# Performance work log

Measured on AMD Instinct MI355X. Metric: run time of the kernel, lower is better.

## Reference

```python
import jax, jax.numpy as jnp
import numpy as np

N, V, E = 65536, 2048, 1024
TEMPERATURE = 0.5
EPS = 1e-10
LOG_PARAM_Q = -2.995732273553991


def _l2_normalize(x, axis):
    # matches torch F.normalize(p=2): x / max(||x||, 1e-12)
    n = jnp.sqrt(jnp.sum(x * x, axis=axis, keepdims=True))
    return x / jnp.maximum(n, 1e-12)


def setup_inputs() -> dict:
    key = jax.random.key(0)
    k1, k2, k3 = jax.random.split(key, 3)
    z = jax.random.normal(k1, (N, E), dtype=jnp.float32)
    emb_weight = jax.random.normal(k2, (V, E), dtype=jnp.float32)
    U = jax.random.uniform(k3, (N, V), dtype=jnp.float32)
    return {"z": z, "emb_weight": emb_weight, "U": U}


def reference(z, emb_weight, U):
    kappa_q = jnp.exp(jnp.float32(LOG_PARAM_Q)) + jnp.float32(1.0)
    zn = _l2_normalize(z, axis=1)              # [N, E]
    emb = _l2_normalize(emb_weight, axis=1)    # [V, E]
    # logit = -distances = kappa_q * z @ emb.T
    logit = kappa_q * jnp.matmul(zn, emb.T)    # [N, V]
    # gumbel-softmax sample (training branch)
    g = -jnp.log(-jnp.log(U + EPS) + EPS)
    tokens = jax.nn.softmax((logit + g) / TEMPERATURE, axis=-1)  # [N, V]
    z_q = jnp.matmul(tokens, emb)              # [N, E]
    return (tokens, z_q)
```

## Files before the change

kernel.cpp:

```cpp
#include <hip/hip_runtime.h>
#include <hip/hip_bf16.h>
#include <stdint.h>

typedef short bf16x8 __attribute__((ext_vector_type(8)));
typedef float floatx4 __attribute__((ext_vector_type(4)));

#define N_ROWS 65536
#define V_DIM 2048
#define E_DIM 1024

__device__ __forceinline__ short f2bf(float x) {
  union { float f; uint32_t u; } c; c.f = x;
  uint32_t r = (c.u + 0x7FFFu + ((c.u >> 16) & 1u)) >> 16;
  return (short)(uint16_t)r;
}
__device__ __forceinline__ float bf16f(short b) {
  union { uint32_t u; float f; } c; c.u = ((uint32_t)(uint16_t)b) << 16;
  return c.f;
}

__device__ __forceinline__ float wave_sum(float v) {
#pragma unroll
  for (int o = 32; o > 0; o >>= 1) v += __shfl_xor(v, o);
  return v;
}
__device__ __forceinline__ float wave_max(float v) {
#pragma unroll
  for (int o = 32; o > 0; o >>= 1) v = fmaxf(v, __shfl_xor(v, o));
  return v;
}

__device__ __forceinline__ void gll16(const short* g, short* l) {
  __builtin_amdgcn_global_load_lds(
      (const __attribute__((address_space(1))) void*)g,
      (__attribute__((address_space(3))) void*)l, 16, 0, 0);
}

#define FRAG(base, R, c) \
  (*(const bf16x8*)((const char*)(base) + ((R) << 7) + (((((c) >> 3) ^ ((R) & 7))) << 4)))

__global__ __launch_bounds__(256) void k_norm_emb(const float* __restrict__ W,
                                                  short* __restrict__ embn,
                                                  short* __restrict__ embnT) {
  const int v = blockIdx.x;
  const int t = threadIdx.x;
  const int w = t >> 6, l = t & 63;
  const float4 val = *(const float4*)&W[(size_t)v * E_DIM + t * 4];
  float ss = val.x * val.x + val.y * val.y + val.z * val.z + val.w * val.w;
  ss = wave_sum(ss);
  __shared__ float red[4];
  if (l == 0) red[w] = ss;
  __syncthreads();
  ss = red[0] + red[1] + red[2] + red[3];
  const float inv = 1.0f / fmaxf(sqrtf(ss), 1e-12f);
  short4 o;
  o.x = f2bf(val.x * inv);
  o.y = f2bf(val.y * inv);
  o.z = f2bf(val.z * inv);
  o.w = f2bf(val.w * inv);
  *(short4*)&embn[(size_t)v * E_DIM + t * 4] = o;
  embnT[(size_t)(t * 4 + 0) * V_DIM + v] = o.x;
  embnT[(size_t)(t * 4 + 1) * V_DIM + v] = o.y;
  embnT[(size_t)(t * 4 + 2) * V_DIM + v] = o.z;
  embnT[(size_t)(t * 4 + 3) * V_DIM + v] = o.w;
}

__global__ __launch_bounds__(256) void k_norm_z(const float* __restrict__ Z,
                                                short* __restrict__ zn) {
  const int w = threadIdx.x >> 6, l = threadIdx.x & 63;
  const int row = blockIdx.x * 4 + w;
  const float* zr = Z + (size_t)row * E_DIM;
  float4 v[4];
  float ss = 0.f;
#pragma unroll
  for (int i = 0; i < 4; ++i) {
    v[i] = *(const float4*)&zr[(i * 64 + l) * 4];
    ss += v[i].x * v[i].x + v[i].y * v[i].y + v[i].z * v[i].z + v[i].w * v[i].w;
  }
  ss = wave_sum(ss);
  const float SCALE = 2.0f * (expf(-2.995732273553991f) + 1.0f);
  const float inv = SCALE / fmaxf(sqrtf(ss), 1e-12f);
  short* zo = zn + (size_t)row * E_DIM;
#pragma unroll
  for (int i = 0; i < 4; ++i) {
    short4 o;
    o.x = f2bf(v[i].x * inv);
    o.y = f2bf(v[i].y * inv);
    o.z = f2bf(v[i].z * inv);
    o.w = f2bf(v[i].w * inv);
    *(short4*)&zo[(i * 64 + l) * 4] = o;
  }
}

template <int KDIM, int NBX, int EPI>
__global__ __launch_bounds__(512, 2) void k_gemm8(
    const short* __restrict__ A, const short* __restrict__ B,
    const float* __restrict__ U, short* __restrict__ Pb,
    float* __restrict__ partials, const float* __restrict__ invsum,
    float* __restrict__ C, float* __restrict__ tokens, int cpx) {
  __shared__ __align__(16) short Sm[65536];
  const int NT = KDIM / 32;
  const int tid = threadIdx.x;
  const int wv = tid >> 6, lane = tid & 63;
  const int lr = lane & 15, lh = lane >> 4;
  const int wr = wv >> 2, wc = wv & 3;
  const int d = blockIdx.x;
  const int L = (d & 7) * cpx + (d >> 3);
  const int by = (EPI == 0) ? (L / NBX) : (L & 255);
  const int bx = (EPI == 0) ? (L % NBX) : (L >> 8);
  const int m0 = by * 256, n0 = bx * 256;
  const int sg = (((lane & 3) ^ ((lane >> 2) & 3) ^ ((lane >> 4) & 3)) << 3);
  const int srow = wv * 16 + (lane >> 2);
  const short* gA = A + (size_t)(m0 + srow) * KDIM + sg;
  const short* gB = B + (size_t)(n0 + srow) * KDIM + sg;
  const int fslot = lh ^ ((lr ^ (lr >> 2)) & 3);
  const int aoff = wr * 8192 + lr * 64 + fslot * 16;
  const int boff = wc * 4096 + lr * 64 + fslot * 16;

#pragma unroll
  for (int t = 0; t < 2; ++t) {
#pragma unroll
    for (int q = 0; q < 2; ++q) {
      gll16(gA + (size_t)(q * 128) * KDIM + t * 32, Sm + t * 8192 + q * 4096 + wv * 512);
      gll16(gB + (size_t)(q * 128) * KDIM + t * 32, Sm + 32768 + t * 8192 + q * 4096 + wv * 512);
    }
  }
  asm volatile("s_waitcnt vmcnt(4)" ::: "memory");
  __builtin_amdgcn_s_barrier();
  __builtin_amdgcn_sched_barrier(0);

  floatx4 acc[8][4] = {};

#define DO_TILE(KT, STAGE, VMN)                                                     \
  {                                                                                 \
    const int cb_ = (KT) & 3;                                                       \
    const char* Ab_ = (const char*)Sm + cb_ * 16384;                                \
    const char* Bb_ = (const char*)Sm + 65536 + cb_ * 16384;                        \
    short* An_ = Sm + (((KT) + 2) & 3) * 8192;                                      \
    short* Bn_ = Sm + 32768 + (((KT) + 2) & 3) * 8192;                              \
    const size_t kc_ = (size_t)((KT) + 2) * 32;                                     \
    bf16x8 bfr[4], af[4];                                                           \
     \
    _Pragma("unroll")                                                               \
    for (int n = 0; n < 4; ++n) bfr[n] = *(const bf16x8*)(Bb_ + boff + n * 1024);   \
    _Pragma("unroll")                                                               \
    for (int i = 0; i < 4; ++i) af[i] = *(const bf16x8*)(Ab_ + aoff + i * 1024);    \
    if (STAGE) {                                                                    \
      gll16(gA + kc_, An_ + wv * 512);                                              \
      gll16(gA + (size_t)128 * KDIM + kc_, An_ + 4096 + wv * 512);                  \
    }                                                                               \
    __builtin_amdgcn_s_barrier();                                                   \
    asm volatile("s_waitcnt lgkmcnt(0)" ::: "memory");                              \
    __builtin_amdgcn_sched_barrier(0);                                              \
    __builtin_amdgcn_s_setprio(1);                                                  \
    _Pragma("unroll")                                                               \
    for (int i = 0; i < 4; ++i) {                                                   \
      _Pragma("unroll")                                                             \
      for (int n = 0; n < 4; ++n)                                                   \
        acc[i][n] =                                                                 \
            __builtin_amdgcn_mfma_f32_16x16x32_bf16(af[i], bfr[n], acc[i][n], 0, 0, 0); \
    }                                                                               \
    __builtin_amdgcn_s_setprio(0);                                                  \
    __builtin_amdgcn_s_barrier();                                                   \
     \
    _Pragma("unroll")                                                               \
    for (int i = 0; i < 4; ++i)                                                     \
      af[i] = *(const bf16x8*)(Ab_ + aoff + 4096 + i * 1024);                       \
    if (STAGE) {                                                                    \
      gll16(gB + kc_, Bn_ + wv * 512);                                              \
      gll16(gB + (size_t)128 * KDIM + kc_, Bn_ + 4096 + wv * 512);                  \
    }                                                                               \
    __builtin_amdgcn_s_barrier();                                                   \
    asm volatile("s_waitcnt lgkmcnt(0)" ::: "memory");                              \
    __builtin_amdgcn_sched_barrier(0);                                              \
    __builtin_amdgcn_s_setprio(1);                                                  \
    _Pragma("unroll")                                                               \
    for (int i = 0; i < 4; ++i) {                                                   \
      _Pragma("unroll")                                                             \
      for (int n = 0; n < 4; ++n)                                                   \
        acc[4 + i][n] =                                                             \
            __builtin_amdgcn_mfma_f32_16x16x32_bf16(af[i], bfr[n], acc[4 + i][n], 0, 0, 0); \
    }                                                                               \
    __builtin_amdgcn_s_setprio(0);                                                  \
    asm volatile("s_waitcnt vmcnt(" #VMN ")" ::: "memory");                         \
    __builtin_amdgcn_s_barrier();                                                   \
    __builtin_amdgcn_sched_barrier(0);                                              \
  }

  for (int kt = 0; kt < NT - 2; ++kt) DO_TILE(kt, 1, 4);
  DO_TILE(NT - 2, 0, 0);
  DO_TILE(NT - 1, 0, 0);
#undef DO_TILE

  const int gr0 = m0 + wr * 128 + lh * 4;
  const int gc0 = n0 + wc * 64 + lr;
  if (EPI == 0) {
    float rs[8][4] = {};
#pragma unroll
    for (int m = 0; m < 8; ++m)
#pragma unroll
      for (int n = 0; n < 4; ++n) {
        const int col = gc0 + n * 16;
#pragma unroll
        for (int j = 0; j < 4; ++j) {
          const int row = gr0 + m * 16 + j;
          const size_t idx = (size_t)row * V_DIM + col;
          const float u = U[idx];
          const float e = __expf(acc[m][n][j] - 2.f * __logf(-__logf(u + 1e-10f) + 1e-10f));
          const short eb = f2bf(e);
          Pb[idx] = eb;
          rs[m][j] += bf16f(eb);
        }
      }
#pragma unroll
    for (int m = 0; m < 8; ++m)
#pragma unroll
      for (int j = 0; j < 4; ++j) {
        float s = rs[m][j];
        s += __shfl_xor(s, 1); s += __shfl_xor(s, 2);
        s += __shfl_xor(s, 4); s += __shfl_xor(s, 8);
        if (lr == 0)
          partials[(size_t)(gr0 + m * 16 + j) * 32 + bx * 4 + wc] = s;
      }
  } else {
#pragma unroll
    for (int m = 0; m < 8; ++m)
#pragma unroll
      for (int j = 0; j < 4; ++j) {
        const int row = gr0 + m * 16 + j;
        const float s = invsum[row];
#pragma unroll
        for (int n = 0; n < 4; ++n)
          C[(size_t)row * E_DIM + gc0 + n * 16] = acc[m][n][j] * s;
      }
    const int tcol0 = bx * 512;
    const int rowoff = tid >> 7;
    const int coff = (tid & 127) * 4;
    for (int it = 0; it < 64; ++it) {
      const int row = m0 + it * 4 + rowoff;
      const float s = invsum[row];
      const short4 pv = *(const short4*)&A[(size_t)row * KDIM + tcol0 + coff];
      float4 o;
      o.x = bf16f(pv.x) * s; o.y = bf16f(pv.y) * s;
      o.z = bf16f(pv.z) * s; o.w = bf16f(pv.w) * s;
      *(float4*)&tokens[(size_t)row * V_DIM + tcol0 + coff] = o;
    }
  }
}

__global__ __launch_bounds__(256) void k_rowsum_inv(const float* __restrict__ partials,
                                                    float* __restrict__ invsum) {
  const int r = blockIdx.x * 256 + threadIdx.x;
  const float4* p = (const float4*)&partials[(size_t)r * 32];
  float s = 0.f;
#pragma unroll
  for (int i = 0; i < 8; ++i) { float4 v = p[i]; s += v.x + v.y + v.z + v.w; }
  invsum[r] = 1.f / s;
}

__global__ __launch_bounds__(256) void k_gemm_nt(const short* __restrict__ A,
                                                 const short* __restrict__ B,
                                                 float* __restrict__ C,
                                                 int lda, int ldb, int ldc, int K) {
  __shared__ __align__(16) short As[128][64];
  __shared__ __align__(16) short Bs[128][64];
  const int t = threadIdx.x;
  const int w = t >> 6, l = t & 63;
  const int lr = l & 15, lh = l >> 4;
  const int m0 = blockIdx.y * 128, n0 = blockIdx.x * 128;
  const int wm = (w >> 1) * 64, wn = (w & 1) * 64;
  floatx4 acc[4][4] = {};
  for (int k0 = 0; k0 < K; k0 += 64) {
    __syncthreads();
#pragma unroll
    for (int i = 0; i < 4; ++i) {
      const int c = i * 256 + t;
      const int r = c >> 3, c8 = (c & 7) * 8;
      *(bf16x8*)&As[r][c8] = *(const bf16x8*)&A[(size_t)(m0 + r) * lda + k0 + c8];
      *(bf16x8*)&Bs[r][c8] = *(const bf16x8*)&B[(size_t)(n0 + r) * ldb + k0 + c8];
    }
    __syncthreads();
#pragma unroll
    for (int kk = 0; kk < 64; kk += 32) {
      bf16x8 af[4], bfr[4];
#pragma unroll
      for (int m = 0; m < 4; ++m) af[m] = *(const bf16x8*)&As[wm + m * 16 + lr][kk + lh * 8];
#pragma unroll
      for (int n = 0; n < 4; ++n) bfr[n] = *(const bf16x8*)&Bs[wn + n * 16 + lr][kk + lh * 8];
#pragma unroll
      for (int m = 0; m < 4; ++m)
#pragma unroll
        for (int n = 0; n < 4; ++n)
          acc[m][n] = __builtin_amdgcn_mfma_f32_16x16x32_bf16(af[m], bfr[n], acc[m][n], 0, 0, 0);
    }
  }
#pragma unroll
  for (int m = 0; m < 4; ++m)
#pragma unroll
    for (int n = 0; n < 4; ++n) {
      const int col = n0 + wn + n * 16 + lr;
#pragma unroll
      for (int j = 0; j < 4; ++j)
        C[(size_t)(m0 + wm + m * 16 + lh * 4 + j) * ldc + col] = acc[m][n][j];
    }
}

__global__ __launch_bounds__(256) void k_gemm_nt_f32a(const float* __restrict__ A,
                                                      const short* __restrict__ B,
                                                      float* __restrict__ C,
                                                      int lda, int ldb, int ldc, int K) {
  __shared__ __align__(16) short As[128][64];
  __shared__ __align__(16) short Bs[128][64];
  const int t = threadIdx.x;
  const int w = t >> 6, l = t & 63;
  const int lr = l & 15, lh = l >> 4;
  const int m0 = blockIdx.y * 128, n0 = blockIdx.x * 128;
  const int wm = (w >> 1) * 64, wn = (w & 1) * 64;
  floatx4 acc[4][4] = {};
  for (int k0 = 0; k0 < K; k0 += 64) {
    __syncthreads();
#pragma unroll
    for (int i = 0; i < 4; ++i) {
      const int c = i * 256 + t;
      const int r = c >> 3, c8 = (c & 7) * 8;
      const float4 a0 = *(const float4*)&A[(size_t)(m0 + r) * lda + k0 + c8];
      const float4 a1 = *(const float4*)&A[(size_t)(m0 + r) * lda + k0 + c8 + 4];
      bf16x8 va;
      va[0] = f2bf(a0.x); va[1] = f2bf(a0.y); va[2] = f2bf(a0.z); va[3] = f2bf(a0.w);
      va[4] = f2bf(a1.x); va[5] = f2bf(a1.y); va[6] = f2bf(a1.z); va[7] = f2bf(a1.w);
      *(bf16x8*)&As[r][c8] = va;
      *(bf16x8*)&Bs[r][c8] = *(const bf16x8*)&B[(size_t)(n0 + r) * ldb + k0 + c8];
    }
    __syncthreads();
#pragma unroll
    for (int kk = 0; kk < 64; kk += 32) {
      bf16x8 af[4], bfr[4];
#pragma unroll
      for (int m = 0; m < 4; ++m) af[m] = *(const bf16x8*)&As[wm + m * 16 + lr][kk + lh * 8];
#pragma unroll
      for (int n = 0; n < 4; ++n) bfr[n] = *(const bf16x8*)&Bs[wn + n * 16 + lr][kk + lh * 8];
#pragma unroll
      for (int m = 0; m < 4; ++m)
#pragma unroll
        for (int n = 0; n < 4; ++n)
          acc[m][n] = __builtin_amdgcn_mfma_f32_16x16x32_bf16(af[m], bfr[n], acc[m][n], 0, 0, 0);
    }
  }
#pragma unroll
  for (int m = 0; m < 4; ++m)
#pragma unroll
    for (int n = 0; n < 4; ++n) {
      const int col = n0 + wn + n * 16 + lr;
#pragma unroll
      for (int j = 0; j < 4; ++j)
        C[(size_t)(m0 + wm + m * 16 + lh * 4 + j) * ldc + col] = acc[m][n][j];
    }
}

__global__ __launch_bounds__(256) void k_gumbel_softmax(float* __restrict__ S,
                                                        const float* __restrict__ U) {
  const int t = threadIdx.x;
  const int w = t >> 6, l = t & 63;
  const size_t base = (size_t)blockIdx.x * V_DIM + t * 8;
  const float4 s0 = *(const float4*)&S[base];
  const float4 s1 = *(const float4*)&S[base + 4];
  const float4 u0 = *(const float4*)&U[base];
  const float4 u1 = *(const float4*)&U[base + 4];
  float x[8];
  x[0] = s0.x - 2.f * __logf(-__logf(u0.x + 1e-10f) + 1e-10f);
  x[1] = s0.y - 2.f * __logf(-__logf(u0.y + 1e-10f) + 1e-10f);
  x[2] = s0.z - 2.f * __logf(-__logf(u0.z + 1e-10f) + 1e-10f);
  x[3] = s0.w - 2.f * __logf(-__logf(u0.w + 1e-10f) + 1e-10f);
  x[4] = s1.x - 2.f * __logf(-__logf(u1.x + 1e-10f) + 1e-10f);
  x[5] = s1.y - 2.f * __logf(-__logf(u1.y + 1e-10f) + 1e-10f);
  x[6] = s1.z - 2.f * __logf(-__logf(u1.z + 1e-10f) + 1e-10f);
  x[7] = s1.w - 2.f * __logf(-__logf(u1.w + 1e-10f) + 1e-10f);
  float lm = x[0];
#pragma unroll
  for (int i = 1; i < 8; ++i) lm = fmaxf(lm, x[i]);
  lm = wave_max(lm);
  __shared__ float redA[4], redB[4];
  if (l == 0) redA[w] = lm;
  __syncthreads();
  const float m = fmaxf(fmaxf(redA[0], redA[1]), fmaxf(redA[2], redA[3]));
  float p[8];
  float ls = 0.f;
#pragma unroll
  for (int i = 0; i < 8; ++i) { p[i] = __expf(x[i] - m); ls += p[i]; }
  ls = wave_sum(ls);
  if (l == 0) redB[w] = ls;
  __syncthreads();
  const float inv = 1.0f / (redB[0] + redB[1] + redB[2] + redB[3]);
  float4 o0 = make_float4(p[0] * inv, p[1] * inv, p[2] * inv, p[3] * inv);
  float4 o1 = make_float4(p[4] * inv, p[5] * inv, p[6] * inv, p[7] * inv);
  *(float4*)&S[base] = o0;
  *(float4*)&S[base + 4] = o1;
}

extern "C" void kernel_launch(void* const* d_in, const int* in_sizes, int n_in,
                              void* d_out, int out_size, void* d_ws, size_t ws_size,
                              hipStream_t stream) {
  const float* z = (const float*)d_in[0];
  const float* W = (const float*)d_in[1];
  const float* U = (const float*)d_in[2];
  float* tokens = (float*)d_out;
  float* zq = tokens + (size_t)N_ROWS * V_DIM;
  short* zn = (short*)zq;

  short* embn = (short*)d_ws;
  short* embnT = embn + (size_t)V_DIM * E_DIM;

  const size_t NEED = (size_t)V_DIM * E_DIM * 2 * 2
                    + (size_t)N_ROWS * 32 * 4
                    + (size_t)N_ROWS * 4
                    + (size_t)N_ROWS * V_DIM * 2;

  k_norm_emb<<<V_DIM, 256, 0, stream>>>(W, embn, embnT);
  k_norm_z<<<N_ROWS / 4, 256, 0, stream>>>(z, zn);

  if (ws_size >= NEED) {
    float* partials = (float*)(embnT + (size_t)V_DIM * E_DIM);
    float* invsum = partials + (size_t)N_ROWS * 32;
    short* Pb = (short*)(invsum + N_ROWS);
    k_gemm8<E_DIM, 8, 0><<<2048, 512, 0, stream>>>(
        zn, embn, U, Pb, partials, nullptr, nullptr, nullptr, 2048 / 8);
    k_rowsum_inv<<<N_ROWS / 256, 256, 0, stream>>>(partials, invsum);
    k_gemm8<V_DIM, 4, 1><<<1024, 512, 0, stream>>>(
        Pb, embnT, nullptr, nullptr, nullptr, invsum, zq, tokens, 1024 / 8);
  } else {
    k_gemm_nt<<<dim3(V_DIM / 128, N_ROWS / 128), 256, 0, stream>>>(
        zn, embn, tokens, E_DIM, E_DIM, V_DIM, E_DIM);
    k_gumbel_softmax<<<N_ROWS, 256, 0, stream>>>(tokens, U);
    k_gemm_nt_f32a<<<dim3(E_DIM / 128, N_ROWS / 128), 256, 0, stream>>>(
        tokens, embnT, zq, V_DIM, V_DIM, E_DIM, V_DIM);
  }
}
```

Baseline: 1.033 ms.

## Write tokens from LDS-staged P tiles inside the second GEMM main loop

The second GEMM (tokens @ emb) previously re-read its bf16 probability tile from global memory in the epilogue to write the normalized fp32 tokens. Now each block writes its share of tokens during the K loop, taking the P fragments already staged in LDS and scaling them by the preloaded inverse row sums. The vmcnt waits are adjusted so the extra stores are counted, and the block index mapping for EPI==1 changes to L/NBX. This removes a redundant global read and overlaps the token stores with MFMA work, at the cost of more complex wait counting and store traffic inside the pipelined loop.

```diff
diff --git a/kernel.cpp b/kernel.cpp
--- a/kernel.cpp
+++ b/kernel.cpp
@@ -35,9 +35,6 @@
       (const __attribute__((address_space(1))) void*)g,
       (__attribute__((address_space(3))) void*)l, 16, 0, 0);
 }
-
-#define FRAG(base, R, c) \
-  (*(const bf16x8*)((const char*)(base) + ((R) << 7) + (((((c) >> 3) ^ ((R) & 7))) << 4)))
 
 __global__ __launch_bounds__(256) void k_norm_emb(const float* __restrict__ W,
                                                   short* __restrict__ embn,
@@ -106,8 +103,7 @@
   const int wr = wv >> 2, wc = wv & 3;
   const int d = blockIdx.x;
   const int L = (d & 7) * cpx + (d >> 3);
-  const int by = (EPI == 0) ? (L / NBX) : (L & 255);
-  const int bx = (EPI == 0) ? (L % NBX) : (L >> 8);
+  const int by = L / NBX, bx = L % NBX;
   const int m0 = by * 256, n0 = bx * 256;
   const int sg = (((lane & 3) ^ ((lane >> 2) & 3) ^ ((lane >> 4) & 3)) << 3);
   const int srow = wv * 16 + (lane >> 2);
@@ -117,6 +113,12 @@
   const int aoff = wr * 8192 + lr * 64 + fslot * 16;
   const int boff = wc * 4096 + lr * 64 + fslot * 16;
 
+  float inv0 = 0.f, inv1 = 0.f;
+  if (EPI == 1) {
+    inv0 = invsum[m0 + srow];
+    inv1 = invsum[m0 + 128 + srow];
+  }
+
 #pragma unroll
   for (int t = 0; t < 2; ++t) {
 #pragma unroll
@@ -131,7 +133,7 @@
 
   floatx4 acc[8][4] = {};
 
-#define DO_TILE(KT, STAGE, VMN)                                                     \
+#define DO_TILE(KT, STAGE, VMN, TOKW_)                                              \
   {                                                                                 \
     const int cb_ = (KT) & 3;                                                       \
     const char* Ab_ = (const char*)Sm + cb_ * 16384;                                \
@@ -182,14 +184,49 @@
             __builtin_amdgcn_mfma_f32_16x16x32_bf16(af[i], bfr[n], acc[4 + i][n], 0, 0, 0); \
     }                                                                               \
     __builtin_amdgcn_s_setprio(0);                                                  \
+    if (TOKW_) {    \
+      const short* myA_ = Sm + cb_ * 8192 + wv * 512 + lane * 8;                    \
+      const bf16x8 v0_ = *(const bf16x8*)myA_;                                      \
+      const bf16x8 v1_ = *(const bf16x8*)(myA_ + 4096);                             \
+      const size_t c0_ = (size_t)(KT) * 32 + sg;                                    \
+      float4 a_, b_;                                                                \
+      a_.x = bf16f(v0_[0]) * inv0; a_.y = bf16f(v0_[1]) * inv0;                     \
+      a_.z = bf16f(v0_[2]) * inv0; a_.w = bf16f(v0_[3]) * inv0;                     \
+      b_.x = bf16f(v0_[4]) * inv0; b_.y = bf16f(v0_[5]) * inv0;                     \
+      b_.z = bf16f(v0_[6]) * inv0; b_.w = bf16f(v0_[7]) * inv0;                     \
+      *(float4*)&tokens[(size_t)(m0 + srow) * KDIM + c0_] = a_;                     \
+      *(float4*)&tokens[(size_t)(m0 + srow) * KDIM + c0_ + 4] = b_;                 \
+      a_.x = bf16f(v1_[0]) * inv1; a_.y = bf16f(v1_[1]) * inv1;                     \
+      a_.z = bf16f(v1_[2]) * inv1; a_.w = bf16f(v1_[3]) * inv1;                     \
+      b_.x = bf16f(v1_[4]) * inv1; b_.y = bf16f(v1_[5]) * inv1;                     \
+      b_.z = bf16f(v1_[6]) * inv1; b_.w = bf16f(v1_[7]) * inv1;                     \
+      *(float4*)&tokens[(size_t)(m0 + 128 + srow) * KDIM + c0_] = a_;               \
+      *(float4*)&tokens[(size_t)(m0 + 128 + srow) * KDIM + c0_ + 4] = b_;           \
+    }                                                                               \
     asm volatile("s_waitcnt vmcnt(" #VMN ")" ::: "memory");                         \
     __builtin_amdgcn_s_barrier();                                                   \
     __builtin_amdgcn_sched_barrier(0);                                              \
   }
 
-  for (int kt = 0; kt < NT - 2; ++kt) DO_TILE(kt, 1, 4);
-  DO_TILE(NT - 2, 0, 0);
-  DO_TILE(NT - 1, 0, 0);
+  if (EPI == 0) {
+    for (int kt = 0; kt < NT - 2; ++kt) DO_TILE(kt, 1, 4, 0);
+    DO_TILE(NT - 2, 0, 0, 0);
+    DO_TILE(NT - 1, 0, 0, 0);
+  } else {
+    const int s = bx * 16;
+    int kt = 0;
+    for (; kt < s; ++kt) DO_TILE(kt, 1, 4, 0);
+    DO_TILE(kt, 1, 8, 1);
+    ++kt;
+    for (; kt < s + 16 && kt < NT - 2; ++kt) DO_TILE(kt, 1, 12, 1);
+    if (kt == s + 16) {
+      DO_TILE(kt, 1, 8, 0);
+      ++kt;
+    }
+    for (; kt < NT - 2; ++kt) DO_TILE(kt, 1, 4, 0);
+    DO_TILE(NT - 2, 0, 0, ((NT - 2) >> 4) == bx);
+    DO_TILE(NT - 1, 0, 0, ((NT - 1) >> 4) == bx);
+  }
 #undef DO_TILE
 
   const int gr0 = m0 + wr * 128 + lh * 4;
@@ -233,18 +270,6 @@
         for (int n = 0; n < 4; ++n)
           C[(size_t)row * E_DIM + gc0 + n * 16] = acc[m][n][j] * s;
       }
-    const int tcol0 = bx * 512;
-    const int rowoff = tid >> 7;
-    const int coff = (tid & 127) * 4;
-    for (int it = 0; it < 64; ++it) {
-      const int row = m0 + it * 4 + rowoff;
-      const float s = invsum[row];
-      const short4 pv = *(const short4*)&A[(size_t)row * KDIM + tcol0 + coff];
-      float4 o;
-      o.x = bf16f(pv.x) * s; o.y = bf16f(pv.y) * s;
-      o.z = bf16f(pv.z) * s; o.w = bf16f(pv.w) * s;
-      *(float4*)&tokens[(size_t)row * V_DIM + tcol0 + coff] = o;
-    }
   }
 }
 
```

After: 926.0 us. 1.12x faster.
